# Kernel optimization log

Hardware: AMD Instinct MI355X
Metric: run time of the kernel (lower is better)

The kernel has to match this reference:

```python
import jax, jax.numpy as jnp
import numpy as np

B, S, D = 2, 2048, 2048
H, H_KV = 16, 4
HD = D // H  # 128
N_REP = H // H_KV
SCALE = HD ** -0.5
NEG = -1e9


def _rope_tables():
    inv_freq = 1.0 / (10000.0 ** (jnp.arange(0, HD, 2, dtype=jnp.float32) / HD))
    t = jnp.arange(S, dtype=jnp.float32)
    freqs = jnp.outer(t, inv_freq)                      # [S, HD/2]
    emb = jnp.concatenate([freqs, freqs], axis=-1)      # [S, HD]
    cos = jnp.broadcast_to(jnp.cos(emb)[None], (B, S, HD))
    sin = jnp.broadcast_to(jnp.sin(emb)[None], (B, S, HD))
    return cos, sin


def setup_inputs() -> dict:
    key = jax.random.key(0)
    ks = jax.random.split(key, 6)
    x = jax.random.normal(ks[0], (B, S, D), dtype=jnp.float32)
    cos, sin = _rope_tables()
    causal = jnp.tril(jnp.ones((S, S), dtype=bool))
    attention_mask = jnp.where(causal, 0.0, NEG).astype(jnp.float32)[None, None]  # [1,1,S,S]
    attention_mask = jnp.broadcast_to(attention_mask, (B, 1, S, S))
    s = 0.02
    Wq = jax.random.normal(ks[1], (D, H * HD), dtype=jnp.float32) * s
    Wk = jax.random.normal(ks[2], (D, H_KV * HD), dtype=jnp.float32) * s
    Wv = jax.random.normal(ks[3], (D, H_KV * HD), dtype=jnp.float32) * s
    Wo = jax.random.normal(ks[4], (H * HD, D), dtype=jnp.float32) * s
    return {"x": x, "cos": cos, "sin": sin, "attention_mask": attention_mask,
            "Wq": Wq, "Wk": Wk, "Wv": Wv, "Wo": Wo}


def _rotate_half(t):
    t1, t2 = t[..., : HD // 2], t[..., HD // 2:]
    return jnp.concatenate([-t2, t1], axis=-1)


def reference(x, cos, sin, attention_mask, Wq, Wk, Wv, Wo):
    b, s = x.shape[:2]
    q = (x @ Wq).reshape(b, s, H, HD).transpose(0, 2, 1, 3)      # [B,H,S,HD]
    k = (x @ Wk).reshape(b, s, H_KV, HD).transpose(0, 2, 1, 3)   # [B,Hkv,S,HD]
    v = (x @ Wv).reshape(b, s, H_KV, HD).transpose(0, 2, 1, 3)
    c = cos[:, None]   # unsqueeze_dim=1 -> [B,1,S,HD]
    sn = sin[:, None]
    q = q * c + _rotate_half(q) * sn
    k = k * c + _rotate_half(k) * sn
    k = jnp.repeat(k, N_REP, axis=1)                              # [B,H,S,HD]
    v = jnp.repeat(v, N_REP, axis=1)
    attn = jnp.einsum('bhqd,bhkd->bhqk', q, k) * SCALE
    attn = attn + attention_mask[:, :, :, : k.shape[-2]]
    attn = jax.nn.softmax(attn, axis=-1)                          # dropout p=0
    out = jnp.einsum('bhqk,bhkd->bhqd', attn, v)
    out = out.transpose(0, 2, 1, 3).reshape(b, s, H * HD)
    out = out @ Wo
    return out, attn
```

## Files before the change

### kernel.cpp

```cpp
#include <hip/hip_runtime.h>

#define B_   2
#define S_   2048
#define D_   2048
#define H_   16
#define HKV_ 4
#define HD_  128
#define SCALE_ 0.08838834764831845f
#define EXPC_ 0.12751746f

typedef unsigned short u16;
typedef unsigned int u32;
typedef __attribute__((ext_vector_type(4))) float  f32x4;
typedef __attribute__((ext_vector_type(8))) __bf16 bf16x8;
typedef __attribute__((ext_vector_type(8))) unsigned short u16x8;

__device__ __forceinline__ u16 f2b(float f) {
  u32 u = __builtin_bit_cast(u32, f);
  u += 0x7fffu + ((u >> 16) & 1u);
  return (u16)(u >> 16);
}
__device__ __forceinline__ float b2f(u16 v) {
  return __builtin_bit_cast(float, (u32)v << 16);
}

__global__ void k_f2b(const float* __restrict__ in, u16* __restrict__ out,
                      u32* __restrict__ knm) {
  if (blockIdx.x == 0 && threadIdx.x < 8) knm[threadIdx.x] = 0u;
  size_t i = (size_t)blockIdx.x * 256 + threadIdx.x;
  float4 v = reinterpret_cast<const float4*>(in)[i];
  ushort4 o;
  o.x = f2b(v.x); o.y = f2b(v.y); o.z = f2b(v.z); o.w = f2b(v.w);
  reinterpret_cast<ushort4*>(out)[i] = o;
}

__global__ void k_wTall(const float* __restrict__ W0, const float* __restrict__ W1,
                        const float* __restrict__ W2, const float* __restrict__ W3,
                        u16* __restrict__ T0, u16* __restrict__ T1,
                        u16* __restrict__ T2, u16* __restrict__ T3) {
  __shared__ float t[32][33];
  const int z = blockIdx.z;
  const float* W = (z == 0) ? W0 : (z == 1) ? W1 : (z == 2) ? W2 : W3;
  u16* T = (z == 0) ? T0 : (z == 1) ? T1 : (z == 2) ? T2 : T3;
  const int N = (z == 0 || z == 3) ? 2048 : 512;
  const int K = 2048;
  int n0 = blockIdx.x * 32, k0 = blockIdx.y * 32;
  if (n0 >= N) return;
  int tx = threadIdx.x, ty = threadIdx.y;
  for (int j = ty; j < 32; j += 8)
    t[j][tx] = W[(size_t)(k0 + j) * N + n0 + tx];
  __syncthreads();
  for (int j = ty; j < 32; j += 8)
    T[(size_t)(n0 + j) * K + k0 + tx] = f2b(t[tx][j]);
}

__global__ __launch_bounds__(256, 3)
void k_gemm(const u16* __restrict__ A, const u16* __restrict__ Bt,
            float* __restrict__ C, int M, int N, int K) {
  __shared__ char smem[128 * 128 + 128 * 128];
  char* As = smem;
  char* Bs = smem + 128 * 128;
  const int tid = threadIdx.x;
  const int lane = tid & 63, wave = tid >> 6;
  const int l16 = lane & 15, lhi = lane >> 4;
  const int wm = (wave >> 1) * 64, wn = (wave & 1) * 64;
  const int bm = blockIdx.y, bn = blockIdx.x;
  const u16* Ab = A + (size_t)bm * 128 * K;
  const u16* Bb = Bt + (size_t)bn * 128 * K;
  f32x4 acc[4][4] = {};
  for (int k0 = 0; k0 < K; k0 += 64) {
    for (int p = 0; p < 4; ++p) {
      int r0 = wave * 32 + p * 8;
      int row = r0 + (lane >> 3);
      int src_off = ((lane & 7) * 16) ^ ((row & 7) << 4);
      const char* ga = (const char*)(Ab + (size_t)row * K + k0) + src_off;
      const char* gb = (const char*)(Bb + (size_t)row * K + k0) + src_off;
      __builtin_amdgcn_global_load_lds(
          (const __attribute__((address_space(1))) void*)ga,
          (__attribute__((address_space(3))) void*)(As + r0 * 128), 16, 0, 0);
      __builtin_amdgcn_global_load_lds(
          (const __attribute__((address_space(1))) void*)gb,
          (__attribute__((address_space(3))) void*)(Bs + r0 * 128), 16, 0, 0);
    }
    __syncthreads();
    for (int ks = 0; ks < 2; ++ks) {
      bf16x8 af[4], bfr[4];
      for (int f = 0; f < 4; ++f) {
        int m = wm + f * 16 + l16;
        af[f] = *reinterpret_cast<const bf16x8*>(As + m * 128 + ((ks * 64 + lhi * 16) ^ ((m & 7) << 4)));
        int n = wn + f * 16 + l16;
        bfr[f] = *reinterpret_cast<const bf16x8*>(Bs + n * 128 + ((ks * 64 + lhi * 16) ^ ((n & 7) << 4)));
      }
      for (int i = 0; i < 4; ++i)
        for (int j = 0; j < 4; ++j)
          acc[i][j] = __builtin_amdgcn_mfma_f32_16x16x32_bf16(af[i], bfr[j], acc[i][j], 0, 0, 0);
    }
    __syncthreads();
  }
  for (int ch = 0; ch < 2; ++ch) {
    __syncthreads();
    if ((wave & 1) == ch) {
      #pragma unroll
      for (int i = 0; i < 4; ++i)
        #pragma unroll
        for (int j = 0; j < 4; ++j)
          #pragma unroll
          for (int r = 0; r < 4; ++r) {
            int lrow = wm + i * 16 + lhi * 4 + r;
            int lcol = j * 16 + l16;
            *reinterpret_cast<float*>(smem + (size_t)(lrow * 64 + lcol) * 4) = acc[i][j][r];
          }
    }
    __syncthreads();
    int rbase = wave * 32 + (lane >> 3);
    int c0 = (lane & 7) * 8;
    #pragma unroll
    for (int i = 0; i < 4; ++i) {
      int rr = rbase + 8 * i;
      const float* src = reinterpret_cast<const float*>(smem + (size_t)(rr * 64 + c0) * 4);
      float4 w0 = *reinterpret_cast<const float4*>(src);
      float4 w1 = *reinterpret_cast<const float4*>(src + 4);
      float* dst = C + (size_t)(bm * 128 + rr) * N + bn * 128 + ch * 64 + c0;
      *reinterpret_cast<float4*>(dst)     = w0;
      *reinterpret_cast<float4*>(dst + 4) = w1;
    }
  }
}

__global__ __launch_bounds__(256, 3)
void k_gemmqkv(const u16* __restrict__ A, const u16* __restrict__ Bt,
               const float* __restrict__ cosT, const float* __restrict__ sinT,
               u16* __restrict__ qb, u16* __restrict__ kb, u16* __restrict__ vT,
               float* __restrict__ qn, u32* __restrict__ knm) {
  __shared__ char smem[33024];
  char* As = smem;
  char* Bs = smem + 16384;
  const int K = 2048;
  const int tid = threadIdx.x;
  const int lane = tid & 63, wave = tid >> 6;
  const int l16 = lane & 15, lhi = lane >> 4;
  const int wm = (wave >> 1) * 64, wn = (wave & 1) * 64;
  const int bm = blockIdx.y, bn = blockIdx.x;
  const u16* Ab = A + (size_t)bm * 128 * K;
  const u16* Bb = Bt + (size_t)bn * 128 * K;
  f32x4 acc[4][4] = {};
  for (int k0 = 0; k0 < K; k0 += 64) {
    for (int p = 0; p < 4; ++p) {
      int r0 = wave * 32 + p * 8;
      int row = r0 + (lane >> 3);
      int src_off = ((lane & 7) * 16) ^ ((row & 7) << 4);
      const char* ga = (const char*)(Ab + (size_t)row * K + k0) + src_off;
      const char* gb = (const char*)(Bb + (size_t)row * K + k0) + src_off;
      __builtin_amdgcn_global_load_lds(
          (const __attribute__((address_space(1))) void*)ga,
          (__attribute__((address_space(3))) void*)(As + r0 * 128), 16, 0, 0);
      __builtin_amdgcn_global_load_lds(
          (const __attribute__((address_space(1))) void*)gb,
          (__attribute__((address_space(3))) void*)(Bs + r0 * 128), 16, 0, 0);
    }
    __syncthreads();
    for (int ks = 0; ks < 2; ++ks) {
      bf16x8 af[4], bfr[4];
      for (int f = 0; f < 4; ++f) {
        int m = wm + f * 16 + l16;
        af[f] = *reinterpret_cast<const bf16x8*>(As + m * 128 + ((ks * 64 + lhi * 16) ^ ((m & 7) << 4)));
        int n = wn + f * 16 + l16;
        bfr[f] = *reinterpret_cast<const bf16x8*>(Bs + n * 128 + ((ks * 64 + lhi * 16) ^ ((n & 7) << 4)));
      }
      for (int i = 0; i < 4; ++i)
        for (int j = 0; j < 4; ++j)
          acc[i][j] = __builtin_amdgcn_mfma_f32_16x16x32_bf16(af[i], bfr[j], acc[i][j], 0, 0, 0);
    }
    __syncthreads();
  }

  const int b = (bm * 128) >> 11;
  const int srow0 = (bm * 128) & 2047;

  if (bn < 20) {
    const bool isq = (bn < 16);
    const int h = isq ? bn : bn - 16;
    u16* outb = isq ? (qb + ((size_t)(b * H_ + h) * S_) * HD_)
                    : (kb + ((size_t)(b * HKV_ + h) * S_) * HD_);
    float* lds = reinterpret_cast<float*>(smem);
    for (int ph = 0; ph < 2; ++ph) {
      __syncthreads();
      if ((wave >> 1) == ph) {
        #pragma unroll
        for (int i = 0; i < 4; ++i)
          #pragma unroll
          for (int j = 0; j < 4; ++j)
            #pragma unroll
            for (int r = 0; r < 4; ++r)
              lds[(i * 16 + lhi * 4 + r) * 129 + wn + j * 16 + l16] = acc[i][j][r];
      }
      __syncthreads();
      const int lrow = tid >> 2, part = tid & 3;
      const int grow = bm * 128 + ph * 64 + lrow;
      const int s = srow0 + ph * 64 + lrow;
      const float* cr = cosT + (size_t)grow * HD_;
      const float* sr = sinT + (size_t)grow * HD_;
      const float* src = lds + lrow * 129;
      u16x8 a0, a1, b0, b1;
      float nrm = 0.f;
      #pragma unroll
      for (int dd = 0; dd < 16; ++dd) {
        int d = part * 16 + dd;
        float v1 = src[d], v2 = src[d + 64];
        float o1 = v1 * cr[d] - v2 * sr[d];
        float o2 = v2 * cr[d + 64] + v1 * sr[d + 64];
        nrm += v1 * v1 + v2 * v2;
        if (dd < 8) { a0[dd] = f2b(o1); b0[dd] = f2b(o2); }
        else        { a1[dd - 8] = f2b(o1); b1[dd - 8] = f2b(o2); }
      }
      u16* orow = outb + (size_t)s * HD_;
      *reinterpret_cast<u16x8*>(orow + part * 16)          = a0;
      *reinterpret_cast<u16x8*>(orow + part * 16 + 8)      = a1;
      *reinterpret_cast<u16x8*>(orow + 64 + part * 16)     = b0;
      *reinterpret_cast<u16x8*>(orow + 64 + part * 16 + 8) = b1;
      nrm += __shfl_xor(nrm, 1);
      nrm += __shfl_xor(nrm, 2);
      if (part == 0) {
        if (isq) qn[((size_t)b * H_ + h) * S_ + s] = sqrtf(nrm);
        else     atomicMax(&knm[b * HKV_ + h], __builtin_bit_cast(u32, nrm));
      }
    }
  } else {
    const int hk = bn - 20;
    u16* vbase = vT + ((size_t)(b * HKV_ + hk) * HD_) * S_;
    #pragma unroll
    for (int i = 0; i < 4; ++i)
      #pragma unroll
      for (int j = 0; j < 4; ++j) {
        int d = wn + j * 16 + l16;
        int s = srow0 + wm + i * 16 + lhi * 4;
        u32 lo = (u32)f2b(acc[i][j][0]) | ((u32)f2b(acc[i][j][1]) << 16);
        u32 hi = (u32)f2b(acc[i][j][2]) | ((u32)f2b(acc[i][j][3]) << 16);
        *reinterpret_cast<uint2*>(vbase + (size_t)d * S_ + s) = make_uint2(lo, hi);
      }
  }
}

__device__ __forceinline__ void map_block(int bid, int& qbi, int& bh) {
  int hi = bid >> 8, lo = bid & 255;
  qbi = hi ? 15 - (lo & 15) : (lo & 15);
  bh = ((lo >> 4) << 1) | hi;
}

__global__ __launch_bounds__(256, 2)
void k_fused(const u16* __restrict__ qb_, const u16* __restrict__ kb_,
             const u16* __restrict__ vT, const float* __restrict__ qn,
             const u32* __restrict__ knm,
             float* __restrict__ attn, u16* __restrict__ oh) {
  __shared__ char Ks[2][16384];
  __shared__ char Vs[2][16384];
  __shared__ char Ps[4][4096];
  const int tid = threadIdx.x;
  const int lane = tid & 63, wave = tid >> 6;
  const int l16 = lane & 15, lhi = lane >> 4;
  const int wq = wave * 32;
  int qbi, bh;
  map_block(blockIdx.x, qbi, bh);
  const int b = bh >> 4, h = bh & 15, hk = h >> 2;
  const int q0 = qbi * 128, kend = q0 + 128;
  const int nt = kend >> 6;

  const u16* Q  = qb_ + ((size_t)(b * H_ + h) * S_ + q0) * HD_;
  const u16* K  = kb_ + (size_t)(b * HKV_ + hk) * S_ * HD_;
  const u16* Vt = vT + (size_t)(b * HKV_ + hk) * HD_ * S_;
  float* attnp = attn + ((size_t)bh * S_ + q0) * S_;
  char* psw = Ps[wave];

  bf16x8 qf[2][4];
  #pragma unroll
  for (int m = 0; m < 2; ++m) {
    const u16* qrow = Q + (size_t)(wq + 16 * m + l16) * HD_ + lhi * 8;
    #pragma unroll
    for (int kd = 0; kd < 4; ++kd)
      qf[m][kd] = *reinterpret_cast<const bf16x8*>(qrow + kd * 32);
  }
  const float kmax = sqrtf(__builtin_bit_cast(float, knm[b * HKV_ + hk]));
  float m2[2];
  #pragma unroll
  for (int m = 0; m < 2; ++m)
    m2[m] = EXPC_ * kmax * qn[(size_t)(b * H_ + h) * S_ + q0 + wq + 16 * m + l16];

  auto STAGE_K = [&](int buf, int kt) {
    #pragma unroll
    for (int p = 0; p < 4; ++p) {
      int row = 16 * wave + p * 4 + (lane >> 4);
      int src = ((lane & 15) * 16) ^ ((row & 7) << 4);
      __builtin_amdgcn_global_load_lds(
          (const __attribute__((address_space(1))) void*)((const char*)(K + (size_t)(kt + row) * HD_) + src),
          (__attribute__((address_space(3))) void*)(Ks[buf] + 4096 * wave + p * 1024), 16, 0, 0);
    }
  };
  auto STAGE_V = [&](int buf, int kt) {
    #pragma unroll
    for (int p = 0; p < 4; ++p) {
      int row = 32 * wave + p * 8 + (lane >> 3);
      int src = ((lane & 7) * 16) ^ ((row & 7) << 4);
      __builtin_amdgcn_global_load_lds(
          (const __attribute__((address_space(1))) void*)((const char*)(Vt + (size_t)row * S_ + kt) + src),
          (__attribute__((address_space(3))) void*)(Vs[buf] + 4096 * wave + p * 1024), 16, 0, 0);
    }
  };

  float rs[2] = {0.f, 0.f};
  STAGE_K(0, 0);
  asm volatile("s_waitcnt vmcnt(0)" ::: "memory");
  __builtin_amdgcn_s_barrier();
  for (int t = 0; t < nt; ++t) {
    const int kt = t * 64, cur = t & 1;
    if (t + 1 < nt) {
      STAGE_K(cur ^ 1, kt + 64);
      asm volatile("s_waitcnt vmcnt(4)" ::: "memory");
    } else {
      asm volatile("s_waitcnt vmcnt(0)" ::: "memory");
    }
    __builtin_amdgcn_sched_barrier(0);
    __builtin_amdgcn_s_barrier();

    f32x4 sacc[2][4] = {};
    __builtin_amdgcn_s_setprio(1);
    #pragma unroll
    for (int kd = 0; kd < 4; ++kd) {
      bf16x8 kf[4];
      #pragma unroll
      for (int n = 0; n < 4; ++n) {
        int krow = 16 * n + l16;
        kf[n] = *reinterpret_cast<const bf16x8*>(Ks[cur] + krow * 256 + ((kd * 64 + lhi * 16) ^ ((krow & 7) << 4)));
      }
      #pragma unroll
      for (int m = 0; m < 2; ++m)
        #pragma unroll
        for (int n = 0; n < 4; ++n)
          sacc[m][n] = __builtin_amdgcn_mfma_f32_16x16x32_bf16(kf[n], qf[m][kd], sacc[m][n], 0, 0, 0);
    }
    __builtin_amdgcn_s_setprio(0);
    const bool mk = (kt + 63 > q0 + wq);
    #pragma unroll
    for (int m = 0; m < 2; ++m)
      #pragma unroll
      for (int n = 0; n < 4; ++n)
        #pragma unroll
        for (int r = 0; r < 4; ++r) {
          float p = exp2f(sacc[m][n][r] * EXPC_ - m2[m]);
          if (mk && (kt + 16 * n + 4 * lhi + r > q0 + wq + 16 * m + l16)) p = 0.f;
          rs[m] += p;
        }
    __builtin_amdgcn_s_barrier();
  }

  STAGE_K(0, 0);
  STAGE_V(0, 0);

  float c2[2];
  #pragma unroll
  for (int m = 0; m < 2; ++m) {
    float s = rs[m];
    s += __shfl_xor(s, 16);
    s += __shfl_xor(s, 32);
    c2[m] = -m2[m] - __log2f(s);
  }

  asm volatile("s_waitcnt vmcnt(0)" ::: "memory");
  __builtin_amdgcn_s_barrier();

  f32x4 oacc[2][8] = {};
  for (int t = 0; t < nt; ++t) {
    const int kt = t * 64, cur = t & 1;
    const bool last = (t == nt - 1);
    if (!last) {
      STAGE_K(cur ^ 1, kt + 64);
      STAGE_V(cur ^ 1, kt + 64);
      asm volatile("s_waitcnt vmcnt(16)" ::: "memory");
    } else {
      asm volatile("s_waitcnt vmcnt(8)" ::: "memory");
    }
    __builtin_amdgcn_sched_barrier(0);
    __builtin_amdgcn_s_barrier();

    f32x4 sacc[2][4] = {};
    __builtin_amdgcn_s_setprio(1);
    #pragma unroll
    for (int kd = 0; kd < 4; ++kd) {
      bf16x8 kf[4];
      #pragma unroll
      for (int n = 0; n < 4; ++n) {
        int krow = 16 * n + l16;
        kf[n] = *reinterpret_cast<const bf16x8*>(Ks[cur] + krow * 256 + ((kd * 64 + lhi * 16) ^ ((krow & 7) << 4)));
      }
      #pragma unroll
      for (int m = 0; m < 2; ++m)
        #pragma unroll
        for (int n = 0; n < 4; ++n)
          sacc[m][n] = __builtin_amdgcn_mfma_f32_16x16x32_bf16(kf[n], qf[m][kd], sacc[m][n], 0, 0, 0);
    }
    __builtin_amdgcn_s_setprio(0);

    const bool mk = (kt + 63 > q0 + wq);
    #pragma unroll
    for (int m = 0; m < 2; ++m) {
      const int lq = 16 * m + l16;
      #pragma unroll
      for (int n = 0; n < 4; ++n) {
        float p[4];
        #pragma unroll
        for (int r = 0; r < 4; ++r) {
          float v = exp2f(sacc[m][n][r] * EXPC_ + c2[m]);
          if (mk && (kt + 16 * n + 4 * lhi + r > q0 + wq + lq)) v = 0.f;
          p[r] = v;
        }
        u32 lo = (u32)f2b(p[0]) | ((u32)f2b(p[1]) << 16);
        u32 hi = (u32)f2b(p[2]) | ((u32)f2b(p[3]) << 16);
        char* ad = psw + lq * 128 + (((16 * n + 4 * lhi) * 2) ^ ((lq & 7) << 4));
        *reinterpret_cast<uint2*>(ad) = make_uint2(lo, hi);
      }
    }

    __builtin_amdgcn_s_setprio(1);
    #pragma unroll
    for (int ks = 0; ks < 2; ++ks) {
      bf16x8 pa[2];
      #pragma unroll
      for (int m = 0; m < 2; ++m) {
        int prow = 16 * m + l16;
        pa[m] = *reinterpret_cast<const bf16x8*>(psw + prow * 128 + ((ks * 64 + lhi * 16) ^ ((prow & 7) << 4)));
      }
      #pragma unroll
      for (int n = 0; n < 8; ++n) {
        int drow = 16 * n + l16;
        bf16x8 vf = *reinterpret_cast<const bf16x8*>(Vs[cur] + drow * 128 + ((ks * 64 + lhi * 16) ^ ((drow & 7) << 4)));
        #pragma unroll
        for (int m = 0; m < 2; ++m)
          oacc[m][n] = __builtin_amdgcn_mfma_f32_16x16x32_bf16(pa[m], vf, oacc[m][n], 0, 0, 0);
      }
    }
    __builtin_amdgcn_s_setprio(0);

    {
      int row = lane >> 3;
      int c0 = (lane & 7) * 8;
      #pragma unroll
      for (int i = 0; i < 4; ++i) {
        int rr = row + 8 * i;
        bf16x8 pv8 = *reinterpret_cast<const bf16x8*>(psw + rr * 128 + ((c0 * 2) ^ ((rr & 7) << 4)));
        const u16* pu = reinterpret_cast<const u16*>(&pv8);
        float4 w0, w1;
        w0.x = b2f(pu[0]); w0.y = b2f(pu[1]); w0.z = b2f(pu[2]); w0.w = b2f(pu[3]);
        w1.x = b2f(pu[4]); w1.y = b2f(pu[5]); w1.z = b2f(pu[6]); w1.w = b2f(pu[7]);
        float* dst = attnp + (size_t)(wq + rr) * S_ + kt + c0;
        *reinterpret_cast<float4*>(dst)     = w0;
        *reinterpret_cast<float4*>(dst + 4) = w1;
      }
    }

    asm volatile("s_waitcnt lgkmcnt(0)" ::: "memory");
    __builtin_amdgcn_sched_barrier(0);
    __builtin_amdgcn_s_barrier();
  }

  char* obase = (wave < 2) ? (Ks[0] + 8192 * wave) : (Vs[0] + 8192 * (wave - 2));
  #pragma unroll
  for (int m = 0; m < 2; ++m)
    #pragma unroll
    for (int n = 0; n < 8; ++n)
      #pragma unroll
      for (int r = 0; r < 4; ++r) {
        int lrow = 16 * m + 4 * lhi + r;
        int col = 16 * n + l16;
        *reinterpret_cast<u16*>(obase + lrow * 256 + col * 2) = f2b(oacc[m][n][r]);
      }
  {
    #pragma unroll
    for (int i = 0; i < 8; ++i) {
      int rr = 4 * i + (lane >> 4);
      bf16x8 v = *reinterpret_cast<const bf16x8*>(obase + rr * 256 + (lane & 15) * 16);
      *reinterpret_cast<bf16x8*>(oh + ((size_t)b * S_ + q0 + wq + rr) * (H_ * HD_) + h * HD_ + (lane & 15) * 8) = v;
    }
  }

  {
    f32x4 z = {0.f, 0.f, 0.f, 0.f};
    for (int row = wave; row < 128; row += 4)
      for (int c = kend + lane * 4; c < S_; c += 256)
        *reinterpret_cast<f32x4*>(attnp + (size_t)row * S_ + c) = z;
  }
}

extern "C" void kernel_launch(void* const* d_in, const int* in_sizes, int n_in,
                              void* d_out, int out_size, void* d_ws, size_t ws_size,
                              hipStream_t stream) {
  const float* x    = (const float*)d_in[0];
  const float* cosT = (const float*)d_in[1];
  const float* sinT = (const float*)d_in[2];
  const float* Wq = (const float*)d_in[4];
  const float* Wk = (const float*)d_in[5];
  const float* Wv = (const float*)d_in[6];
  const float* Wo = (const float*)d_in[7];
  float* out  = (float*)d_out;
  float* attn = out + (size_t)B_ * S_ * D_;

  char* ws = (char*)d_ws;
  u16*   xb     = (u16*)(ws);
  u16*   wqkvT  = (u16*)(ws + 16777216);
  u16*   woT    = (u16*)(ws + 29360128);
  float* qn     = (float*)(ws + 37748736);
  u16*   qb     = (u16*)(ws + 88080384);
  u16*   kb     = (u16*)(ws + 104857600);
  u16*   vT     = (u16*)(ws + 109051904);
  u16*   oh     = (u16*)(ws + 113246208);
  u32*   knm    = (u32*)(ws + 130023424);

  k_f2b<<<8192, 256, 0, stream>>>(x, xb, knm);
  k_wTall<<<dim3(64, 64, 4), dim3(32, 8), 0, stream>>>(
      Wq, Wk, Wv, Wo,
      wqkvT, wqkvT + (size_t)2048 * 2048, wqkvT + (size_t)2560 * 2048, woT);

  k_gemmqkv<<<dim3(24, 32), 256, 0, stream>>>(xb, wqkvT, cosT, sinT,
                                              qb, kb, vT, qn, knm);

  k_fused<<<512, 256, 0, stream>>>(qb, kb, vT, qn, knm, attn, oh);

  k_gemm<<<dim3(16, 32), 256, 0, stream>>>(oh, woT, out, 4096, 2048, 2048);
}
```

Before: 336.7 us.

## Merge prep kernels and iterate attention PV pass in reverse tile order

Folds the x-to-bf16 conversion into the weight transpose kernel as an extra grid slice, which removes one kernel launch. In the attention kernel, the second pass now walks KV tiles from last to first. The first V tile is staged before the row-sum reduction, and the tile the previous pass already holds in the current K buffer is reused, so the upfront full vmcnt(0) wait and one K stage are dropped. This relies on the K buffer still holding the last tile from the first pass, and it changes the summation order of the output.

Result: faster. 324.6 us (-3.6%).

```diff
diff --git a/kernel.cpp b/kernel.cpp
--- a/kernel.cpp
+++ b/kernel.cpp
@@ -24,29 +24,34 @@
   return __builtin_bit_cast(float, (u32)v << 16);
 }
 
-__global__ void k_f2b(const float* __restrict__ in, u16* __restrict__ out,
-                      u32* __restrict__ knm) {
-  if (blockIdx.x == 0 && threadIdx.x < 8) knm[threadIdx.x] = 0u;
-  size_t i = (size_t)blockIdx.x * 256 + threadIdx.x;
-  float4 v = reinterpret_cast<const float4*>(in)[i];
-  ushort4 o;
-  o.x = f2b(v.x); o.y = f2b(v.y); o.z = f2b(v.z); o.w = f2b(v.w);
-  reinterpret_cast<ushort4*>(out)[i] = o;
-}
-
-__global__ void k_wTall(const float* __restrict__ W0, const float* __restrict__ W1,
-                        const float* __restrict__ W2, const float* __restrict__ W3,
-                        u16* __restrict__ T0, u16* __restrict__ T1,
-                        u16* __restrict__ T2, u16* __restrict__ T3) {
+__global__ void k_prep(const float* __restrict__ x, const float* __restrict__ W0,
+                       const float* __restrict__ W1, const float* __restrict__ W2,
+                       const float* __restrict__ W3,
+                       u16* __restrict__ xb, u16* __restrict__ T0, u16* __restrict__ T1,
+                       u16* __restrict__ T2, u16* __restrict__ T3, u32* __restrict__ knm) {
+  const int z = blockIdx.z;
+  const int tx = threadIdx.x, ty = threadIdx.y;
+  if (z == 4) {
+    const int flat = blockIdx.y * 64 + blockIdx.x;
+    const int tid = ty * 32 + tx;
+    if (flat == 0 && tid < 8) knm[tid] = 0u;
+    #pragma unroll
+    for (int hh = 0; hh < 2; ++hh) {
+      size_t q = (size_t)flat * 512 + hh * 256 + tid;
+      float4 v = reinterpret_cast<const float4*>(x)[q];
+      ushort4 o;
+      o.x = f2b(v.x); o.y = f2b(v.y); o.z = f2b(v.z); o.w = f2b(v.w);
+      reinterpret_cast<ushort4*>(xb)[q] = o;
+    }
+    return;
+  }
   __shared__ float t[32][33];
-  const int z = blockIdx.z;
   const float* W = (z == 0) ? W0 : (z == 1) ? W1 : (z == 2) ? W2 : W3;
   u16* T = (z == 0) ? T0 : (z == 1) ? T1 : (z == 2) ? T2 : T3;
   const int N = (z == 0 || z == 3) ? 2048 : 512;
   const int K = 2048;
   int n0 = blockIdx.x * 32, k0 = blockIdx.y * 32;
   if (n0 >= N) return;
-  int tx = threadIdx.x, ty = threadIdx.y;
   for (int j = ty; j < 32; j += 8)
     t[j][tx] = W[(size_t)(k0 + j) * N + n0 + tx];
   __syncthreads();
@@ -352,8 +357,7 @@
     __builtin_amdgcn_s_barrier();
   }
 
-  STAGE_K(0, 0);
-  STAGE_V(0, 0);
+  STAGE_V((nt - 1) & 1, (nt - 1) * 64);
 
   float c2[2];
   #pragma unroll
@@ -364,17 +368,17 @@
     c2[m] = -m2[m] - __log2f(s);
   }
 
-  asm volatile("s_waitcnt vmcnt(0)" ::: "memory");
-  __builtin_amdgcn_s_barrier();
-
   f32x4 oacc[2][8] = {};
-  for (int t = 0; t < nt; ++t) {
+  for (int t = nt - 1; t >= 0; --t) {
     const int kt = t * 64, cur = t & 1;
-    const bool last = (t == nt - 1);
-    if (!last) {
-      STAGE_K(cur ^ 1, kt + 64);
-      STAGE_V(cur ^ 1, kt + 64);
-      asm volatile("s_waitcnt vmcnt(16)" ::: "memory");
+    if (t > 0) {
+      STAGE_K(cur ^ 1, kt - 64);
+      STAGE_V(cur ^ 1, kt - 64);
+      if (t == nt - 1) {
+        asm volatile("s_waitcnt vmcnt(8)" ::: "memory");
+      } else {
+        asm volatile("s_waitcnt vmcnt(16)" ::: "memory");
+      }
     } else {
       asm volatile("s_waitcnt vmcnt(8)" ::: "memory");
     }
@@ -513,10 +517,9 @@
   u16*   oh     = (u16*)(ws + 113246208);
   u32*   knm    = (u32*)(ws + 130023424);
 
-  k_f2b<<<8192, 256, 0, stream>>>(x, xb, knm);
-  k_wTall<<<dim3(64, 64, 4), dim3(32, 8), 0, stream>>>(
-      Wq, Wk, Wv, Wo,
-      wqkvT, wqkvT + (size_t)2048 * 2048, wqkvT + (size_t)2560 * 2048, woT);
+  k_prep<<<dim3(64, 64, 5), dim3(32, 8), 0, stream>>>(
+      x, Wq, Wk, Wv, Wo, xb,
+      wqkvT, wqkvT + (size_t)2048 * 2048, wqkvT + (size_t)2560 * 2048, woT, knm);
 
   k_gemmqkv<<<dim3(24, 32), 256, 0, stream>>>(xb, wqkvT, cosT, sinT,
                                               qb, kb, vT, qn, knm);
```
